# Kernel optimization log

Hardware: AMD Instinct MI355X
Metric: run time of the kernel (lower is better)

The kernel has to match this reference:

```python
import jax, jax.numpy as jnp
import numpy as np

N_ENTITIES = 100000
EMBED_DIM = 128
N_EDGES = 1600000
LEAKY_SLOPE = 0.01  # nn.LeakyReLU default


def setup_inputs() -> dict:
    key = jax.random.key(0)
    k1, k2, k3, k4, k5, k6, k7, k8 = jax.random.split(key, 8)
    entity_embs = jax.random.normal(k1, (N_ENTITIES, EMBED_DIM), dtype=jnp.float32)
    adj_rows = jax.random.randint(k2, (N_EDGES,), 0, N_ENTITIES, dtype=jnp.int32)
    adj_cols = jax.random.randint(k3, (N_EDGES,), 0, N_ENTITIES, dtype=jnp.int32)
    adj_vals = jax.random.uniform(k4, (N_EDGES,), dtype=jnp.float32)
    s = 1.0 / np.sqrt(EMBED_DIM)  # nn.Linear default init scale
    W_self = jax.random.uniform(k5, (EMBED_DIM, EMBED_DIM), jnp.float32, -s, s)
    b_self = jax.random.uniform(k6, (EMBED_DIM,), jnp.float32, -s, s)
    W_neigh = jax.random.uniform(k7, (EMBED_DIM, EMBED_DIM), jnp.float32, -s, s)
    b_neigh = jax.random.uniform(k8, (EMBED_DIM,), jnp.float32, -s, s)
    return {"entity_embs": entity_embs, "adj_rows": adj_rows, "adj_cols": adj_cols,
            "adj_vals": adj_vals, "W_self": W_self, "b_self": b_self,
            "W_neigh": W_neigh, "b_neigh": b_neigh}


def reference(entity_embs, adj_rows, adj_cols, adj_vals, W_self, b_self, W_neigh, b_neigh):
    # self path: Linear(input_dim, output_dim) -> x @ W.T + b
    self_emb = entity_embs @ W_self.T + b_self  # [N, D]
    # neighbor path: sparse adjacency SpMM (COO): out[r] += v * embs[c]
    contrib = adj_vals[:, None] * entity_embs[adj_cols]  # [E, D]
    neigh = jax.ops.segment_sum(contrib, adj_rows, num_segments=N_ENTITIES)  # [N, D]
    neigh_emb = neigh @ W_neigh.T + b_neigh
    out = jax.nn.leaky_relu(self_emb + neigh_emb, negative_slope=LEAKY_SLOPE)
    # dropout is identity in eval mode
    return out
```

## Files before the change

### kernel.cpp

```cpp
#include <hip/hip_runtime.h>

#define DIM 128
#define TILE_R 32
#define CAP 64

typedef __attribute__((ext_vector_type(8))) short short8;
typedef __attribute__((ext_vector_type(4))) float floatx4;

static __device__ __forceinline__ short f2bf(float x) {
    unsigned u = __float_as_uint(x);
    u = (u + 0x7FFF + ((u >> 16) & 1)) >> 16;
    return (short)u;
}
static __device__ __forceinline__ float bflo(unsigned p) { return __uint_as_float(p << 16); }
static __device__ __forceinline__ float bfhi(unsigned p) { return __uint_as_float(p & 0xFFFF0000u); }

static __device__ __forceinline__ unsigned packcv(int c, float v) {
    int q = (int)(v * 32768.f + 0.5f);
    q = q > 32767 ? 32767 : q;
    return ((unsigned)c << 15) | (unsigned)q;
}

__global__ __launch_bounds__(256) void zero_kernel(float4* __restrict__ out, int n4) {
    int i = blockIdx.x * 256 + threadIdx.x;
    if (i < n4) out[i] = make_float4(0.f, 0.f, 0.f, 0.f);
}

__global__ __launch_bounds__(256) void zero_counts_kernel(int* __restrict__ cnt,
                                                          int* __restrict__ cursor, int n) {
    int i = blockIdx.x * 256 + threadIdx.x;
    if (i < n) cnt[i] = 0;
    if (i == 0) *cursor = 0;
}

__global__ __launch_bounds__(256) void prep_kernel(const float* __restrict__ Wself,
                                                   const float* __restrict__ Wneigh,
                                                   short* __restrict__ Wf,
                                                   int* __restrict__ next, int nRows) {
    int idx = blockIdx.x * 256 + threadIdx.x;
    if (idx < 4096) {
        int t = idx >> 8;
        int s = (idx >> 6) & 3;
        int lane = idx & 63;
        int n = (t & 7) * 16 + (lane & 15);
        int k0 = s * 32 + (lane >> 4) * 8;
        const float* row = (t < 8 ? Wself : Wneigh) + (size_t)n * DIM + k0;
        short8 v;
#pragma unroll
        for (int j = 0; j < 8; j++) v[j] = f2bf(row[j]);
        *(short8*)(Wf + (size_t)idx * 8) = v;
    }
    int r = idx - 4096;
    if (r >= 0 && r < nRows) next[r] = r * CAP;
}

__global__ __launch_bounds__(256) void fill1_kernel(const int* __restrict__ rows,
                                                    const int* __restrict__ cols,
                                                    const float* __restrict__ vals,
                                                    int* __restrict__ next,
                                                    unsigned* __restrict__ pk, int nE) {
    int i4 = (blockIdx.x * 256 + threadIdx.x) * 4;
    if (i4 + 3 < nE) {
        int4 r = *(const int4*)(rows + i4);
        int4 c = *(const int4*)(cols + i4);
        float4 v = *(const float4*)(vals + i4);
        unsigned q0 = packcv(c.x, v.x), q1 = packcv(c.y, v.y);
        unsigned q2 = packcv(c.z, v.z), q3 = packcv(c.w, v.w);
        int p0 = atomicAdd(&next[r.x], 1);
        int p1 = atomicAdd(&next[r.y], 1);
        int p2 = atomicAdd(&next[r.z], 1);
        int p3 = atomicAdd(&next[r.w], 1);
        if (p0 < r.x * CAP + CAP) pk[p0] = q0;
        if (p1 < r.y * CAP + CAP) pk[p1] = q1;
        if (p2 < r.z * CAP + CAP) pk[p2] = q2;
        if (p3 < r.w * CAP + CAP) pk[p3] = q3;
    } else {
        for (int k = 0; k < 4 && i4 + k < nE; k++) {
            int rr = rows[i4 + k];
            unsigned q = packcv(cols[i4 + k], vals[i4 + k]);
            int p = atomicAdd(&next[rr], 1);
            if (p < rr * CAP + CAP) pk[p] = q;
        }
    }
}

__global__ __launch_bounds__(256) void hist_kernel(const int* __restrict__ rows,
                                                   int* __restrict__ cnt, int nE) {
    int i4 = (blockIdx.x * 256 + threadIdx.x) * 4;
    if (i4 + 3 < nE) {
        int4 r = *(const int4*)(rows + i4);
        atomicAdd(&cnt[r.x], 1);
        atomicAdd(&cnt[r.y], 1);
        atomicAdd(&cnt[r.z], 1);
        atomicAdd(&cnt[r.w], 1);
    } else {
        for (int k = 0; k < 4 && i4 + k < nE; k++) atomicAdd(&cnt[rows[i4 + k]], 1);
    }
}

__global__ __launch_bounds__(256) void offsets_kernel(int* __restrict__ next,
                                                      int* __restrict__ start,
                                                      int* __restrict__ cursor, int n) {
    int i = blockIdx.x * 256 + threadIdx.x;
    int lane = threadIdx.x & 63;
    int c = (i < n) ? next[i] : 0;
    int s = c;
#pragma unroll
    for (int d = 1; d < 64; d <<= 1) {
        int t = __shfl_up(s, d);
        if (lane >= d) s += t;
    }
    int total = __shfl(s, 63);
    int base = 0;
    if (lane == 63) base = atomicAdd(cursor, total);
    base = __shfl(base, 63);
    int off = base + s - c;
    if (i < n) {
        start[i] = off;
        next[i] = off;
    }
}

__global__ __launch_bounds__(256) void fillB_kernel(const int* __restrict__ rows,
                                                    const int* __restrict__ cols,
                                                    const float* __restrict__ vals,
                                                    int* __restrict__ next,
                                                    int2* __restrict__ csr, int nE) {
    int i4 = (blockIdx.x * 256 + threadIdx.x) * 4;
    if (i4 + 3 < nE) {
        int4 r = *(const int4*)(rows + i4);
        int4 c = *(const int4*)(cols + i4);
        float4 v = *(const float4*)(vals + i4);
        int p0 = atomicAdd(&next[r.x], 1);
        int p1 = atomicAdd(&next[r.y], 1);
        int p2 = atomicAdd(&next[r.z], 1);
        int p3 = atomicAdd(&next[r.w], 1);
        csr[p0] = make_int2(c.x, __float_as_int(v.x));
        csr[p1] = make_int2(c.y, __float_as_int(v.y));
        csr[p2] = make_int2(c.z, __float_as_int(v.z));
        csr[p3] = make_int2(c.w, __float_as_int(v.w));
    } else {
        for (int k = 0; k < 4 && i4 + k < nE; k++) {
            int p = atomicAdd(&next[rows[i4 + k]], 1);
            csr[p] = make_int2(cols[i4 + k], __float_as_int(vals[i4 + k]));
        }
    }
}

__global__ __launch_bounds__(256) void wprep_kernel(const float* __restrict__ Wself,
                                                    const float* __restrict__ Wneigh,
                                                    short* __restrict__ Wf) {
    int idx = blockIdx.x * 256 + threadIdx.x;
    int t = idx >> 8;
    int s = (idx >> 6) & 3;
    int lane = idx & 63;
    int n = (t & 7) * 16 + (lane & 15);
    int k0 = s * 32 + (lane >> 4) * 8;
    const float* row = (t < 8 ? Wself : Wneigh) + (size_t)n * DIM + k0;
    short8 v;
#pragma unroll
    for (int j = 0; j < 8; j++) v[j] = f2bf(row[j]);
    *(short8*)(Wf + (size_t)idx * 8) = v;
}

__global__ __launch_bounds__(256) void gemm_kernel(const float* __restrict__ embs,
                                                   const short* __restrict__ Wf,
                                                   unsigned short* __restrict__ Sb,
                                                   unsigned short* __restrict__ Yb,
                                                   int nRows) {
    __shared__ __align__(16) unsigned short cbuf[4][16][264];
    int wave = threadIdx.x >> 6;
    int lane = threadIdx.x & 63;
    int quad = lane >> 4;
    int m0 = blockIdx.x * 64 + wave * 16;
    int m = m0 + (lane & 15);
    bool valid = m < nRows;

    const float* Arow = embs + (size_t)m * DIM;
    short8 a[4];
#pragma unroll
    for (int s = 0; s < 4; s++) {
        float4 f0 = make_float4(0.f, 0.f, 0.f, 0.f), f1 = f0;
        if (valid) {
            f0 = *(const float4*)(Arow + s * 32 + quad * 8);
            f1 = *(const float4*)(Arow + s * 32 + quad * 8 + 4);
        }
        short8 av;
        av[0] = f2bf(f0.x); av[1] = f2bf(f0.y); av[2] = f2bf(f0.z); av[3] = f2bf(f0.w);
        av[4] = f2bf(f1.x); av[5] = f2bf(f1.y); av[6] = f2bf(f1.z); av[7] = f2bf(f1.w);
        a[s] = av;
    }

    const short8* WfV = (const short8*)Wf;
#pragma unroll
    for (int t = 0; t < 16; t++) {
        floatx4 acc = {0.f, 0.f, 0.f, 0.f};
#pragma unroll
        for (int s = 0; s < 4; s++) {
            short8 b = WfV[(t * 4 + s) * 64 + lane];
            acc = __builtin_amdgcn_mfma_f32_16x16x32_bf16(a[s], b, acc, 0, 0, 0);
        }
        int col = t * 16 + (lane & 15);
#pragma unroll
        for (int reg = 0; reg < 4; reg++) {
            cbuf[wave][quad * 4 + reg][col] = (unsigned short)f2bf(acc[reg]);
        }
    }

#pragma unroll
    for (int it = 0; it < 8; it++) {
        int chunk = it * 64 + lane;
        int row = chunk >> 5;
        int off = chunk & 31;
        int colb = off * 8;
        int grow = m0 + row;
        if (grow < nRows) {
            uint4 d = *(const uint4*)&cbuf[wave][row][colb];
            unsigned short* dst = (colb < DIM) ? (Sb + (size_t)grow * DIM + colb)
                                               : (Yb + (size_t)grow * DIM + (colb - DIM));
            *(uint4*)dst = d;
        }
    }
}

__global__ __launch_bounds__(256) void gatherY_pk_kernel(const unsigned* __restrict__ Sb,
                                                         const unsigned* __restrict__ Yb,
                                                         const int* __restrict__ rowEnd,
                                                         const unsigned* __restrict__ pk,
                                                         const float* __restrict__ bself,
                                                         const float* __restrict__ bneigh,
                                                         float* __restrict__ out, int nRows) {
    int r = blockIdx.x * 4 + (threadIdx.x >> 6);
    if (r >= nRows) return;
    int lane = threadIdx.x & 63;
    int s = r * CAP;
    int e = min(__builtin_amdgcn_readfirstlane(rowEnd[r]), s + CAP);
    float ax = 0.f, ay = 0.f;
    const float qs = 1.f / 32768.f;
    int j = s;
    for (; j + 4 <= e; j += 4) {
        uint4 q = *(const uint4*)(pk + j);
        unsigned y0 = Yb[(size_t)(q.x >> 15) * 64 + lane];
        unsigned y1 = Yb[(size_t)(q.y >> 15) * 64 + lane];
        unsigned y2 = Yb[(size_t)(q.z >> 15) * 64 + lane];
        unsigned y3 = Yb[(size_t)(q.w >> 15) * 64 + lane];
        float v0 = (float)(q.x & 32767u) * qs;
        float v1 = (float)(q.y & 32767u) * qs;
        float v2 = (float)(q.z & 32767u) * qs;
        float v3 = (float)(q.w & 32767u) * qs;
        ax += v0 * bflo(y0) + v1 * bflo(y1) + v2 * bflo(y2) + v3 * bflo(y3);
        ay += v0 * bfhi(y0) + v1 * bfhi(y1) + v2 * bfhi(y2) + v3 * bfhi(y3);
    }
    for (; j < e; j++) {
        unsigned q = pk[j];
        float v = (float)(q & 32767u) * qs;
        unsigned y = Yb[(size_t)(q >> 15) * 64 + lane];
        ax += v * bflo(y);
        ay += v * bfhi(y);
    }
    unsigned sp = __builtin_nontemporal_load(&Sb[(size_t)r * 64 + lane]);
    float ox = bflo(sp) + bself[2 * lane] + bneigh[2 * lane] + ax;
    float oy = bfhi(sp) + bself[2 * lane + 1] + bneigh[2 * lane + 1] + ay;
    ox = ox > 0.f ? ox : 0.01f * ox;
    oy = oy > 0.f ? oy : 0.01f * oy;
    union { float2 f; double d; } u;
    u.f = make_float2(ox, oy);
    __builtin_nontemporal_store(u.d, (double*)(out + (size_t)r * DIM + lane * 2));
}

__global__ __launch_bounds__(256) void gatherY_kernel(const unsigned* __restrict__ Sb,
                                                      const unsigned* __restrict__ Yb,
                                                      const int* __restrict__ start,
                                                      const int* __restrict__ next,
                                                      const int2* __restrict__ csr,
                                                      const float* __restrict__ bself,
                                                      const float* __restrict__ bneigh,
                                                      float* __restrict__ out, int nRows) {
    int r = blockIdx.x * 4 + (threadIdx.x >> 6);
    if (r >= nRows) return;
    int lane = threadIdx.x & 63;
    int s = __builtin_amdgcn_readfirstlane(start[r]);
    int e = __builtin_amdgcn_readfirstlane(next[r]);
    float ax = 0.f, ay = 0.f;
    int j = s;
    for (; j + 4 <= e; j += 4) {
        int2 c0 = csr[j], c1 = csr[j + 1], c2 = csr[j + 2], c3 = csr[j + 3];
        unsigned y0 = Yb[(size_t)c0.x * 64 + lane];
        unsigned y1 = Yb[(size_t)c1.x * 64 + lane];
        unsigned y2 = Yb[(size_t)c2.x * 64 + lane];
        unsigned y3 = Yb[(size_t)c3.x * 64 + lane];
        float v0 = __int_as_float(c0.y), v1 = __int_as_float(c1.y);
        float v2 = __int_as_float(c2.y), v3 = __int_as_float(c3.y);
        ax += v0 * bflo(y0) + v1 * bflo(y1) + v2 * bflo(y2) + v3 * bflo(y3);
        ay += v0 * bfhi(y0) + v1 * bfhi(y1) + v2 * bfhi(y2) + v3 * bfhi(y3);
    }
    for (; j < e; j++) {
        int2 c = csr[j];
        float v = __int_as_float(c.y);
        unsigned y = Yb[(size_t)c.x * 64 + lane];
        ax += v * bflo(y);
        ay += v * bfhi(y);
    }
    unsigned sp = __builtin_nontemporal_load(&Sb[(size_t)r * 64 + lane]);
    float ox = bflo(sp) + bself[2 * lane] + bneigh[2 * lane] + ax;
    float oy = bfhi(sp) + bself[2 * lane + 1] + bneigh[2 * lane + 1] + ay;
    ox = ox > 0.f ? ox : 0.01f * ox;
    oy = oy > 0.f ? oy : 0.01f * oy;
    union { float2 f; double d; } u;
    u.f = make_float2(ox, oy);
    __builtin_nontemporal_store(u.d, (double*)(out + (size_t)r * DIM + lane * 2));
}

__global__ __launch_bounds__(256) void gather_embs_kernel(const float2* __restrict__ embs2,
                                                          const int* __restrict__ start,
                                                          const int* __restrict__ next,
                                                          const int2* __restrict__ csr,
                                                          float* __restrict__ out, int nRows) {
    int r = blockIdx.x * 4 + (threadIdx.x >> 6);
    if (r >= nRows) return;
    int lane = threadIdx.x & 63;
    int s = start[r];
    int e = next[r];
    float2 acc = make_float2(0.f, 0.f);
    for (int b = s; b < e; b += 64) {
        int n = min(64, e - b);
        int2 cv = make_int2(0, 0);
        if (lane < n) cv = csr[b + lane];
        float vf = __int_as_float(cv.y);
        for (int j = 0; j < n; j++) {
            int cj = __shfl(cv.x, j);
            float vj = __shfl(vf, j);
            float2 x = embs2[(size_t)cj * 64 + lane];
            acc.x += vj * x.x;
            acc.y += vj * x.y;
        }
    }
    ((float2*)out)[(size_t)r * 64 + lane] = acc;
}

__global__ __launch_bounds__(256) void scatter_kernel(
    const float* __restrict__ embs, const int* __restrict__ rows,
    const int* __restrict__ cols, const float* __restrict__ vals,
    float* __restrict__ out, int nE) {
    int e = blockIdx.x * 4 + (threadIdx.x >> 6);
    if (e >= nE) return;
    int lane = threadIdx.x & 63;
    int r = rows[e];
    int c = cols[e];
    float v = vals[e];
    float2 x = ((const float2*)(embs + (size_t)c * DIM))[lane];
    float* dst = out + (size_t)r * DIM + lane * 2;
    unsafeAtomicAdd(dst, v * x.x);
    unsafeAtomicAdd(dst + 1, v * x.y);
}

__global__ __launch_bounds__(256) void fused_kernel(
    const float* __restrict__ embs, const float* __restrict__ Wself,
    const float* __restrict__ bself, const float* __restrict__ Wneigh,
    const float* __restrict__ bneigh, float* __restrict__ out, int nRows) {
    __shared__ float xs[TILE_R][DIM];
    __shared__ float xn[TILE_R][DIM];

    int r0 = blockIdx.x * TILE_R;
    if (r0 >= nRows) return;

    const float4* gs = (const float4*)(embs + (size_t)r0 * DIM);
    const float4* gn = (const float4*)(out + (size_t)r0 * DIM);
    float4* sxs = (float4*)&xs[0][0];
    float4* sxn = (float4*)&xn[0][0];
    for (int i = threadIdx.x; i < TILE_R * DIM / 4; i += 256) {
        sxs[i] = gs[i];
        sxn[i] = gn[i];
    }
    __syncthreads();

    int j = threadIdx.x & 127;
    int rbase = (threadIdx.x >> 7) * 16;

    const float4* ws = (const float4*)(Wself + (size_t)j * DIM);
    const float4* wn = (const float4*)(Wneigh + (size_t)j * DIM);

    float acc[16];
#pragma unroll
    for (int i = 0; i < 16; i++) acc[i] = 0.f;

    for (int k4 = 0; k4 < DIM / 4; k4++) {
        float4 a = ws[k4];
        float4 b = wn[k4];
#pragma unroll
        for (int rr = 0; rr < 16; rr++) {
            float4 x = *(const float4*)&xs[rbase + rr][k4 * 4];
            float4 y = *(const float4*)&xn[rbase + rr][k4 * 4];
            acc[rr] += x.x * a.x + x.y * a.y + x.z * a.z + x.w * a.w
                     + y.x * b.x + y.y * b.y + y.z * b.z + y.w * b.w;
        }
    }

    float bias = bself[j] + bneigh[j];
#pragma unroll
    for (int rr = 0; rr < 16; rr++) {
        float v = acc[rr] + bias;
        out[(size_t)(r0 + rbase + rr) * DIM + j] = v > 0.f ? v : 0.01f * v;
    }
}

static inline size_t a16(size_t x) { return (x + 15) & ~(size_t)15; }

extern "C" void kernel_launch(void* const* d_in, const int* in_sizes, int n_in,
                              void* d_out, int out_size, void* d_ws, size_t ws_size,
                              hipStream_t stream) {
    const float* embs   = (const float*)d_in[0];
    const int*   rows   = (const int*)d_in[1];
    const int*   cols   = (const int*)d_in[2];
    const float* vals   = (const float*)d_in[3];
    const float* Wself  = (const float*)d_in[4];
    const float* bself  = (const float*)d_in[5];
    const float* Wneigh = (const float*)d_in[6];
    const float* bneigh = (const float*)d_in[7];
    float* out = (float*)d_out;

    int nE = in_sizes[1];
    int nRows = out_size / DIM;
    size_t wfBytes = (size_t)16 * 4 * 64 * 8 * 2;
    size_t bfPlane = (size_t)nRows * DIM * 2;

    size_t A6_next = 0;
    size_t A6_buck = A6_next + a16((size_t)nRows * 4);
    size_t A6_wf   = A6_buck + a16((size_t)nRows * CAP * 4);
    size_t A6_y    = A6_wf + a16(wfBytes);
    size_t A6_s    = A6_y + bfPlane;
    size_t needA6  = A6_s + bfPlane;
    bool   okA6    = nRows <= (1 << 17);

    size_t B_next  = 0;
    size_t B_start = B_next + a16((size_t)nRows * 4);
    size_t B_cur   = B_start + a16((size_t)nRows * 4);
    size_t B_csr   = B_cur + 16;
    size_t B_wf    = B_csr + a16((size_t)nE * 8);
    size_t B_y     = B_wf + a16(wfBytes);
    size_t B_s     = B_y + bfPlane;
    size_t needB   = B_s + bfPlane;

    size_t C_csr  = a16((size_t)(2 * nRows + 1) * 4);
    size_t needC  = C_csr + (size_t)nE * 8;

    int rb = (nRows + 255) / 256;
    int eb4 = (nE / 4 + 255) / 256;
    int ebp = ((nE + 3) / 4 + 255) / 256;

    if (okA6 && ws_size >= needA6) {
        int*      next = (int*)((char*)d_ws + A6_next);
        unsigned* pk   = (unsigned*)((char*)d_ws + A6_buck);
        short*    Wf   = (short*)((char*)d_ws + A6_wf);
        unsigned short* Yb = (unsigned short*)((char*)d_ws + A6_y);
        unsigned short* Sb = (unsigned short*)((char*)d_ws + A6_s);

        prep_kernel<<<(4096 + nRows + 255) / 256, 256, 0, stream>>>(Wself, Wneigh, Wf, next, nRows);
        fill1_kernel<<<ebp, 256, 0, stream>>>(rows, cols, vals, next, pk, nE);
        gemm_kernel<<<(nRows + 63) / 64, 256, 0, stream>>>(embs, Wf, Sb, Yb, nRows);
        gatherY_pk_kernel<<<(nRows + 3) / 4, 256, 0, stream>>>(
            (const unsigned*)Sb, (const unsigned*)Yb, next, pk, bself, bneigh, out, nRows);
    } else if (ws_size >= needB) {
        int*  next   = (int*)((char*)d_ws + B_next);
        int*  start  = (int*)((char*)d_ws + B_start);
        int*  cursor = (int*)((char*)d_ws + B_cur);
        int2* csr    = (int2*)((char*)d_ws + B_csr);
        short* Wf    = (short*)((char*)d_ws + B_wf);
        unsigned short* Yb = (unsigned short*)((char*)d_ws + B_y);
        unsigned short* Sb = (unsigned short*)((char*)d_ws + B_s);

        zero_counts_kernel<<<rb, 256, 0, stream>>>(next, cursor, nRows);
        hist_kernel<<<eb4, 256, 0, stream>>>(rows, next, nE);
        offsets_kernel<<<rb, 256, 0, stream>>>(next, start, cursor, nRows);
        fillB_kernel<<<eb4, 256, 0, stream>>>(rows, cols, vals, next, csr, nE);
        wprep_kernel<<<16, 256, 0, stream>>>(Wself, Wneigh, Wf);
        gemm_kernel<<<(nRows + 63) / 64, 256, 0, stream>>>(embs, Wf, Sb, Yb, nRows);
        gatherY_kernel<<<(nRows + 3) / 4, 256, 0, stream>>>(
            (const unsigned*)Sb, (const unsigned*)Yb, start, next, csr,
            bself, bneigh, out, nRows);
    } else if (ws_size >= needC) {
        int* next = (int*)d_ws;
        int* start = next + nRows;
        int* cursor = start + nRows;
        int2* csr = (int2*)((char*)d_ws + C_csr);

        zero_counts_kernel<<<rb, 256, 0, stream>>>(next, cursor, nRows);
        hist_kernel<<<eb4, 256, 0, stream>>>(rows, next, nE);
        offsets_kernel<<<rb, 256, 0, stream>>>(next, start, cursor, nRows);
        fillB_kernel<<<eb4, 256, 0, stream>>>(rows, cols, vals, next, csr, nE);
        gather_embs_kernel<<<(nRows + 3) / 4, 256, 0, stream>>>(
            (const float2*)embs, start, next, csr, out, nRows);
        fused_kernel<<<(nRows + TILE_R - 1) / TILE_R, 256, 0, stream>>>(
            embs, Wself, bself, Wneigh, bneigh, out, nRows);
    } else {
        int n4 = out_size / 4;
        zero_kernel<<<(n4 + 255) / 256, 256, 0, stream>>>((float4*)out, n4);
        scatter_kernel<<<(nE + 3) / 4, 256, 0, stream>>>(embs, rows, cols, vals, out, nE);
        fused_kernel<<<(nRows + TILE_R - 1) / TILE_R, 256, 0, stream>>>(
            embs, Wself, bself, Wneigh, bneigh, out, nRows);
    }
}
```

Measured before the change: 336.9 us.

## Partition bucket fill by row region per XCD and widen GEMM tiles

Edge packing is split into its own kernel. The bucket fill now runs as NREG×NCHUNK blocks, where each block scans one edge chunk and only applies atomics for rows in its region, so atomics and bucket writes for a row range stay within one XCD's L2. The cost is that every edge's row index is read NREG times. Separately, the GEMM now handles 64 rows per wave, reusing each W fragment across four MFMAs, and drops the LDS staging in favour of direct 2-byte strided global stores, which may coalesce poorly.

```diff
diff --git a/kernel.cpp b/kernel.cpp
--- a/kernel.cpp
+++ b/kernel.cpp
@@ -3,6 +3,8 @@
 #define DIM 128
 #define TILE_R 32
 #define CAP 64
+#define NREG 8
+#define NCHUNK 128
 
 typedef __attribute__((ext_vector_type(8))) short short8;
 typedef __attribute__((ext_vector_type(4))) float floatx4;
@@ -54,32 +56,62 @@
     if (r >= 0 && r < nRows) next[r] = r * CAP;
 }
 
-__global__ __launch_bounds__(256) void fill1_kernel(const int* __restrict__ rows,
-                                                    const int* __restrict__ cols,
-                                                    const float* __restrict__ vals,
-                                                    int* __restrict__ next,
-                                                    unsigned* __restrict__ pk, int nE) {
+__global__ __launch_bounds__(256) void pack_kernel(const int* __restrict__ cols,
+                                                   const float* __restrict__ vals,
+                                                   unsigned* __restrict__ pe, int nE) {
     int i4 = (blockIdx.x * 256 + threadIdx.x) * 4;
     if (i4 + 3 < nE) {
-        int4 r = *(const int4*)(rows + i4);
         int4 c = *(const int4*)(cols + i4);
         float4 v = *(const float4*)(vals + i4);
-        unsigned q0 = packcv(c.x, v.x), q1 = packcv(c.y, v.y);
-        unsigned q2 = packcv(c.z, v.z), q3 = packcv(c.w, v.w);
-        int p0 = atomicAdd(&next[r.x], 1);
-        int p1 = atomicAdd(&next[r.y], 1);
-        int p2 = atomicAdd(&next[r.z], 1);
-        int p3 = atomicAdd(&next[r.w], 1);
-        if (p0 < r.x * CAP + CAP) pk[p0] = q0;
-        if (p1 < r.y * CAP + CAP) pk[p1] = q1;
-        if (p2 < r.z * CAP + CAP) pk[p2] = q2;
-        if (p3 < r.w * CAP + CAP) pk[p3] = q3;
+        uint4 o;
+        o.x = packcv(c.x, v.x);
+        o.y = packcv(c.y, v.y);
+        o.z = packcv(c.z, v.z);
+        o.w = packcv(c.w, v.w);
+        *(uint4*)(pe + i4) = o;
     } else {
-        for (int k = 0; k < 4 && i4 + k < nE; k++) {
-            int rr = rows[i4 + k];
-            unsigned q = packcv(cols[i4 + k], vals[i4 + k]);
-            int p = atomicAdd(&next[rr], 1);
-            if (p < rr * CAP + CAP) pk[p] = q;
+        for (int k = 0; k < 4 && i4 + k < nE; k++) pe[i4 + k] = packcv(cols[i4 + k], vals[i4 + k]);
+    }
+}
+
+__global__ __launch_bounds__(256) void fill_xcd_pk_kernel(const int* __restrict__ rows,
+                                                          const unsigned* __restrict__ pe,
+                                                          int* __restrict__ next,
+                                                          unsigned* __restrict__ pk,
+                                                          int nE, int nRows) {
+    int region = blockIdx.x & (NREG - 1);
+    int chunk = blockIdx.x / NREG;
+    int rowsPerReg = (nRows + NREG - 1) / NREG;
+    int rowLo = region * rowsPerReg;
+    int rowHi = min(rowLo + rowsPerReg, nRows);
+    int per = (nE + NCHUNK - 1) / NCHUNK;
+    per = (per + 3) & ~3;
+    int s = chunk * per;
+    int e = min(s + per, nE);
+
+    for (int base = s + threadIdx.x * 4; base < e; base += 256 * 4) {
+        int r4[4];
+        unsigned p4[4];
+        int cnt = 4;
+        if (base + 3 < e) {
+            int4 rv = *(const int4*)(rows + base);
+            uint4 pv = *(const uint4*)(pe + base);
+            r4[0] = rv.x; r4[1] = rv.y; r4[2] = rv.z; r4[3] = rv.w;
+            p4[0] = pv.x; p4[1] = pv.y; p4[2] = pv.z; p4[3] = pv.w;
+        } else {
+            cnt = e - base;
+            for (int k = 0; k < cnt; k++) {
+                r4[k] = rows[base + k];
+                p4[k] = pe[base + k];
+            }
+        }
+#pragma unroll 4
+        for (int k = 0; k < cnt; k++) {
+            int rr = r4[k];
+            if (rr >= rowLo && rr < rowHi) {
+                int p = atomicAdd(&next[rr], 1);
+                if (p < rr * CAP + CAP) pk[p] = p4[k];
+            }
         }
     }
 }
@@ -163,62 +195,59 @@
     *(short8*)(Wf + (size_t)idx * 8) = v;
 }
 
-__global__ __launch_bounds__(256) void gemm_kernel(const float* __restrict__ embs,
-                                                   const short* __restrict__ Wf,
-                                                   unsigned short* __restrict__ Sb,
-                                                   unsigned short* __restrict__ Yb,
-                                                   int nRows) {
-    __shared__ __align__(16) unsigned short cbuf[4][16][264];
+__global__ __launch_bounds__(256) void gemm4_kernel(const float* __restrict__ embs,
+                                                    const short* __restrict__ Wf,
+                                                    unsigned short* __restrict__ Sb,
+                                                    unsigned short* __restrict__ Yb,
+                                                    int nRows) {
     int wave = threadIdx.x >> 6;
     int lane = threadIdx.x & 63;
     int quad = lane >> 4;
-    int m0 = blockIdx.x * 64 + wave * 16;
-    int m = m0 + (lane & 15);
-    bool valid = m < nRows;
-
-    const float* Arow = embs + (size_t)m * DIM;
-    short8 a[4];
-#pragma unroll
-    for (int s = 0; s < 4; s++) {
-        float4 f0 = make_float4(0.f, 0.f, 0.f, 0.f), f1 = f0;
-        if (valid) {
-            f0 = *(const float4*)(Arow + s * 32 + quad * 8);
-            f1 = *(const float4*)(Arow + s * 32 + quad * 8 + 4);
-        }
-        short8 av;
-        av[0] = f2bf(f0.x); av[1] = f2bf(f0.y); av[2] = f2bf(f0.z); av[3] = f2bf(f0.w);
-        av[4] = f2bf(f1.x); av[5] = f2bf(f1.y); av[6] = f2bf(f1.z); av[7] = f2bf(f1.w);
-        a[s] = av;
+    int m0 = blockIdx.x * 256 + wave * 64;
+
+    short8 a[4][4];
+#pragma unroll
+    for (int rt = 0; rt < 4; rt++) {
+        int m = m0 + rt * 16 + (lane & 15);
+        bool valid = m < nRows;
+        const float* Arow = embs + (size_t)m * DIM;
+#pragma unroll
+        for (int s = 0; s < 4; s++) {
+            float4 f0 = make_float4(0.f, 0.f, 0.f, 0.f), f1 = f0;
+            if (valid) {
+                f0 = *(const float4*)(Arow + s * 32 + quad * 8);
+                f1 = *(const float4*)(Arow + s * 32 + quad * 8 + 4);
+            }
+            short8 av;
+            av[0] = f2bf(f0.x); av[1] = f2bf(f0.y); av[2] = f2bf(f0.z); av[3] = f2bf(f0.w);
+            av[4] = f2bf(f1.x); av[5] = f2bf(f1.y); av[6] = f2bf(f1.z); av[7] = f2bf(f1.w);
+            a[rt][s] = av;
+        }
     }
 
     const short8* WfV = (const short8*)Wf;
 #pragma unroll
     for (int t = 0; t < 16; t++) {
-        floatx4 acc = {0.f, 0.f, 0.f, 0.f};
+        floatx4 acc0 = {0.f, 0.f, 0.f, 0.f};
+        floatx4 acc1 = acc0, acc2 = acc0, acc3 = acc0;
 #pragma unroll
         for (int s = 0; s < 4; s++) {
             short8 b = WfV[(t * 4 + s) * 64 + lane];
-            acc = __builtin_amdgcn_mfma_f32_16x16x32_bf16(a[s], b, acc, 0, 0, 0);
+            acc0 = __builtin_amdgcn_mfma_f32_16x16x32_bf16(a[0][s], b, acc0, 0, 0, 0);
+            acc1 = __builtin_amdgcn_mfma_f32_16x16x32_bf16(a[1][s], b, acc1, 0, 0, 0);
+            acc2 = __builtin_amdgcn_mfma_f32_16x16x32_bf16(a[2][s], b, acc2, 0, 0, 0);
+            acc3 = __builtin_amdgcn_mfma_f32_16x16x32_bf16(a[3][s], b, acc3, 0, 0, 0);
         }
         int col = t * 16 + (lane & 15);
+        unsigned short* dst = (col < DIM) ? (Sb + col) : (Yb + (col - DIM));
 #pragma unroll
         for (int reg = 0; reg < 4; reg++) {
-            cbuf[wave][quad * 4 + reg][col] = (unsigned short)f2bf(acc[reg]);
-        }
-    }
-
-#pragma unroll
-    for (int it = 0; it < 8; it++) {
-        int chunk = it * 64 + lane;
-        int row = chunk >> 5;
-        int off = chunk & 31;
-        int colb = off * 8;
-        int grow = m0 + row;
-        if (grow < nRows) {
-            uint4 d = *(const uint4*)&cbuf[wave][row][colb];
-            unsigned short* dst = (colb < DIM) ? (Sb + (size_t)grow * DIM + colb)
-                                               : (Yb + (size_t)grow * DIM + (colb - DIM));
-            *(uint4*)dst = d;
+            int g0 = m0 + quad * 4 + reg;
+            int g1 = g0 + 16, g2 = g0 + 32, g3 = g0 + 48;
+            if (g0 < nRows) dst[(size_t)g0 * DIM] = (unsigned short)f2bf(acc0[reg]);
+            if (g1 < nRows) dst[(size_t)g1 * DIM] = (unsigned short)f2bf(acc1[reg]);
+            if (g2 < nRows) dst[(size_t)g2 * DIM] = (unsigned short)f2bf(acc2[reg]);
+            if (g3 < nRows) dst[(size_t)g3 * DIM] = (unsigned short)f2bf(acc3[reg]);
         }
     }
 }
@@ -424,13 +453,14 @@
     size_t wfBytes = (size_t)16 * 4 * 64 * 8 * 2;
     size_t bfPlane = (size_t)nRows * DIM * 2;
 
-    size_t A6_next = 0;
-    size_t A6_buck = A6_next + a16((size_t)nRows * 4);
-    size_t A6_wf   = A6_buck + a16((size_t)nRows * CAP * 4);
-    size_t A6_y    = A6_wf + a16(wfBytes);
-    size_t A6_s    = A6_y + bfPlane;
-    size_t needA6  = A6_s + bfPlane;
-    bool   okA6    = nRows <= (1 << 17);
+    size_t A7_next = 0;
+    size_t A7_buck = A7_next + a16((size_t)nRows * 4);
+    size_t A7_pe   = A7_buck + a16((size_t)nRows * CAP * 4);
+    size_t A7_wf   = A7_pe + a16((size_t)nE * 4);
+    size_t A7_y    = A7_wf + a16(wfBytes);
+    size_t A7_s    = A7_y + bfPlane;
+    size_t needA7  = A7_s + bfPlane;
+    bool   okA7    = nRows <= (1 << 17);
 
     size_t B_next  = 0;
     size_t B_start = B_next + a16((size_t)nRows * 4);
@@ -448,16 +478,18 @@
     int eb4 = (nE / 4 + 255) / 256;
     int ebp = ((nE + 3) / 4 + 255) / 256;
 
-    if (okA6 && ws_size >= needA6) {
-        int*      next = (int*)((char*)d_ws + A6_next);
-        unsigned* pk   = (unsigned*)((char*)d_ws + A6_buck);
-        short*    Wf   = (short*)((char*)d_ws + A6_wf);
-        unsigned short* Yb = (unsigned short*)((char*)d_ws + A6_y);
-        unsigned short* Sb = (unsigned short*)((char*)d_ws + A6_s);
+    if (okA7 && ws_size >= needA7) {
+        int*      next = (int*)((char*)d_ws + A7_next);
+        unsigned* pk   = (unsigned*)((char*)d_ws + A7_buck);
+        unsigned* pe   = (unsigned*)((char*)d_ws + A7_pe);
+        short*    Wf   = (short*)((char*)d_ws + A7_wf);
+        unsigned short* Yb = (unsigned short*)((char*)d_ws + A7_y);
+        unsigned short* Sb = (unsigned short*)((char*)d_ws + A7_s);
 
         prep_kernel<<<(4096 + nRows + 255) / 256, 256, 0, stream>>>(Wself, Wneigh, Wf, next, nRows);
-        fill1_kernel<<<ebp, 256, 0, stream>>>(rows, cols, vals, next, pk, nE);
-        gemm_kernel<<<(nRows + 63) / 64, 256, 0, stream>>>(embs, Wf, Sb, Yb, nRows);
+        pack_kernel<<<ebp, 256, 0, stream>>>(cols, vals, pe, nE);
+        fill_xcd_pk_kernel<<<NREG * NCHUNK, 256, 0, stream>>>(rows, pe, next, pk, nE, nRows);
+        gemm4_kernel<<<(nRows + 255) / 256, 256, 0, stream>>>(embs, Wf, Sb, Yb, nRows);
         gatherY_pk_kernel<<<(nRows + 3) / 4, 256, 0, stream>>>(
             (const unsigned*)Sb, (const unsigned*)Yb, next, pk, bself, bneigh, out, nRows);
     } else if (ws_size >= needB) {
@@ -474,7 +506,7 @@
         offsets_kernel<<<rb, 256, 0, stream>>>(next, start, cursor, nRows);
         fillB_kernel<<<eb4, 256, 0, stream>>>(rows, cols, vals, next, csr, nE);
         wprep_kernel<<<16, 256, 0, stream>>>(Wself, Wneigh, Wf);
-        gemm_kernel<<<(nRows + 63) / 64, 256, 0, stream>>>(embs, Wf, Sb, Yb, nRows);
+        gemm4_kernel<<<(nRows + 255) / 256, 256, 0, stream>>>(embs, Wf, Sb, Yb, nRows);
         gatherY_kernel<<<(nRows + 3) / 4, 256, 0, stream>>>(
             (const unsigned*)Sb, (const unsigned*)Yb, start, next, csr,
             bself, bneigh, out, nRows);
```

Result: faster. 297.8 us (-11.6%).
